# Kernel optimization log

Measured on AMD Instinct MI355X. Metric: run time of the kernel, lower is better.

The kernel has to match this reference:

```python
import jax, jax.numpy as jnp
import numpy as np

N_NODES = 50000
N_EDGES = 50000  # per-node attention scores are used as per-hyperedge weights => M == N
IN_CH = 128
OUT_CH = 128
NNZ = 800000


def setup_inputs() -> dict:
    key = jax.random.key(0)
    k = jax.random.split(key, 7)
    x = jax.random.normal(k[0], (N_NODES, IN_CH), dtype=jnp.float32)
    node_idx = jax.random.randint(k[1], (NNZ,), 0, N_NODES)
    edge_idx = jax.random.randint(k[2], (NNZ,), 0, N_EDGES)
    hyperedge_index = jnp.stack([node_idx, edge_idx]).astype(jnp.int64)
    s_in = 1.0 / np.sqrt(IN_CH)
    attn_w = jax.random.uniform(k[3], (1, IN_CH), minval=-s_in, maxval=s_in, dtype=jnp.float32)
    attn_b = jax.random.uniform(k[4], (1,), minval=-s_in, maxval=s_in, dtype=jnp.float32)
    lin_w = jax.random.uniform(k[5], (OUT_CH, IN_CH), minval=-s_in, maxval=s_in, dtype=jnp.float32)
    bias = jax.random.uniform(k[6], (OUT_CH,), minval=-s_in, maxval=s_in, dtype=jnp.float32)
    return {"x": x, "hyperedge_index": hyperedge_index,
            "attn_w": attn_w, "attn_b": attn_b, "lin_w": lin_w, "bias": bias}


def reference(x, hyperedge_index, attn_w, attn_b, lin_w, bias):
    # x: [N, C_in]; hyperedge_index: [2, nnz] (row 0: node ids, row 1: hyperedge ids)
    node_idx = hyperedge_index[0]
    edge_idx = hyperedge_index[1]
    N = x.shape[0]
    M = N_EDGES

    # edge_weight = sigmoid(attn(x)) -> used as hyperedge_weight (per-edge, M == N)
    w = jax.nn.sigmoid(x @ attn_w.T + attn_b)[:, 0]            # [M]

    xl = x @ lin_w.T                                           # [N, C_out]

    # D_v = sum of incident hyperedge weights per node; D^{-1} with inf -> 0
    D = jax.ops.segment_sum(w[edge_idx], node_idx, num_segments=N)
    Dinv = jnp.where(D > 0, 1.0 / D, 0.0)                      # [N]

    # B_e = hyperedge degree; B^{-1} with inf -> 0
    ones = jnp.ones(edge_idx.shape, dtype=x.dtype)
    Bdeg = jax.ops.segment_sum(ones, edge_idx, num_segments=M)
    Binv = jnp.where(Bdeg > 0, 1.0 / Bdeg, 0.0)                # [M]

    # node -> hyperedge: message = B_e^{-1} * x_j, aggregated at edge e
    msg = Binv[edge_idx][:, None] * xl[node_idx]               # [nnz, C_out]
    e_feat = jax.ops.segment_sum(msg, edge_idx, num_segments=M)

    # hyperedge -> node: message = D_v^{-1} * e_feat, aggregated at node v
    out = jax.ops.segment_sum(e_feat[edge_idx], node_idx, num_segments=N)
    out = Dinv[:, None] * out

    return out + bias
```

## Files before the change

### kernel.cpp

```cpp
#include <hip/hip_runtime.h>
#include <math.h>

#define CH 128
#define CAP 64
#define RSB 9
#define RS  (1 << RSB)
#define CAPB 10240
#define PB 2048
#define SUB 16
#define IDS 32

typedef __attribute__((ext_vector_type(8))) short bf16x8;
typedef __attribute__((ext_vector_type(4))) float f32x4;

__device__ __forceinline__ unsigned short f2bf(float f) {
    union { float f; unsigned u; } v; v.f = f;
    unsigned r = v.u + 0x7FFF + ((v.u >> 16) & 1);
    return (unsigned short)(r >> 16);
}
__device__ __forceinline__ float bflo(unsigned u) {
    union { unsigned u; float f; } v; v.u = u << 16; return v.f;
}
__device__ __forceinline__ float bfhi(unsigned u) {
    union { unsigned u; float f; } v; v.u = u & 0xFFFF0000u; return v.f;
}
__device__ __forceinline__ unsigned pack2bf(float a, float b) {
    return (unsigned)f2bf(a) | ((unsigned)f2bf(b) << 16);
}

__global__ __launch_bounds__(256) void fused_main(const float* __restrict__ x,
                                                  const float* __restrict__ attn_w,
                                                  const float* __restrict__ attn_b,
                                                  const float* __restrict__ lw,
                                                  unsigned short* __restrict__ xl,
                                                  float* __restrict__ w,
                                                  int nStrips,
                                                  const int* __restrict__ nidx,
                                                  const int* __restrict__ eidx,
                                                  int* __restrict__ binCnt,
                                                  unsigned int* __restrict__ binData,
                                                  int nnz, int nbd, int SB) {
    __shared__ unsigned short wl[128 * 136];
    __shared__ float awl[128];
    if ((int)blockIdx.x < SB) {
        int* hist = (int*)wl;
        int* base = ((int*)wl) + 256;
        int nbt = 2 * nbd;
        for (int i = threadIdx.x; i < nbt; i += 256) hist[i] = 0;
        __syncthreads();
        int k0 = blockIdx.x * PB + threadIdx.x;
        int vv[8], ee[8], sE[8], sN[8];
#pragma unroll
        for (int u = 0; u < 8; ++u) {
            int k = k0 + u * 256;
            if (k < nnz) {
                int v = nidx[k], e = eidx[k];
                vv[u] = v; ee[u] = e;
                sE[u] = atomicAdd(&hist[e >> RSB], 1);
                sN[u] = atomicAdd(&hist[nbd + (v >> RSB)], 1);
            } else vv[u] = -1;
        }
        __syncthreads();
        for (int i = threadIdx.x; i < nbt; i += 256)
            if (hist[i]) base[i] = atomicAdd(&binCnt[i], hist[i]);
        __syncthreads();
#pragma unroll
        for (int u = 0; u < 8; ++u) {
            if (vv[u] < 0) continue;
            int bE = ee[u] >> RSB;
            int bN = nbd + (vv[u] >> RSB);
            int iE = min(base[bE] + sE[u], CAPB - 1);
            int iN = min(base[bN] + sN[u], CAPB - 1);
            binData[(size_t)bE * CAPB + iE] = ((unsigned)ee[u] << 16) | (unsigned)vv[u];
            binData[(size_t)bN * CAPB + iN] = ((unsigned)vv[u] << 16) | (unsigned)ee[u];
        }
        return;
    }
    int tid = threadIdx.x;
    for (int i = tid; i < 2048; i += 256) {
        float4 vlo = ((const float4*)lw)[2 * i];
        float4 vhi = ((const float4*)lw)[2 * i + 1];
        int4 dst;
        dst.x = (int)pack2bf(vlo.x, vlo.y);
        dst.y = (int)pack2bf(vlo.z, vlo.w);
        dst.z = (int)pack2bf(vhi.x, vhi.y);
        dst.w = (int)pack2bf(vhi.z, vhi.w);
        *(int4*)(wl + (i >> 4) * 136 + (i & 15) * 8) = dst;
    }
    if (tid < 128) awl[tid] = attn_w[tid];
    float ab = attn_b[0];
    __syncthreads();
    int gb = blockIdx.x - SB;
    int wid = (gb << 2) | (tid >> 6);
    int lane = tid & 63;
    int m = lane & 15, quad = lane >> 4;
    int nWaves = ((int)gridDim.x - SB) << 2;
    for (int s = wid; s < nStrips; s += nWaves) {
        int r0 = s << 4;
        const float* xr = x + (size_t)(r0 + m) * CH + quad * 8;
        float att = 0.f;
        bf16x8 a0, a1, a2, a3;
#define LOAD_FRAG(AFRAG, F)                                                   \
        {                                                                     \
            float4 lo = *(const float4*)(xr + (F) * 32);                      \
            float4 hi = *(const float4*)(xr + (F) * 32 + 4);                  \
            const float* ap = &awl[(F) * 32 + quad * 8];                      \
            att += lo.x * ap[0] + lo.y * ap[1] + lo.z * ap[2] + lo.w * ap[3]  \
                 + hi.x * ap[4] + hi.y * ap[5] + hi.z * ap[6] + hi.w * ap[7]; \
            union { int4 i; bf16x8 v; } pk;                                   \
            pk.i.x = (int)pack2bf(lo.x, lo.y);                                \
            pk.i.y = (int)pack2bf(lo.z, lo.w);                                \
            pk.i.z = (int)pack2bf(hi.x, hi.y);                                \
            pk.i.w = (int)pack2bf(hi.z, hi.w);                                \
            AFRAG = pk.v;                                                     \
        }
        LOAD_FRAG(a0, 0)
        LOAD_FRAG(a1, 1)
        LOAD_FRAG(a2, 2)
        LOAD_FRAG(a3, 3)
#undef LOAD_FRAG
        att += __shfl_xor(att, 16, 64);
        att += __shfl_xor(att, 32, 64);
        if (quad == 0) w[r0 + m] = 1.0f / (1.0f + expf(-(att + ab)));
        unsigned short* orow = xl + (size_t)(r0 + quad * 4) * CH + m;
#pragma unroll
        for (int c0 = 0; c0 < 128; c0 += 16) {
            const unsigned short* wr = wl + (c0 + m) * 136 + quad * 8;
            f32x4 acc = {0.f, 0.f, 0.f, 0.f};
            acc = __builtin_amdgcn_mfma_f32_16x16x32_bf16(a0, *(const bf16x8*)(wr), acc, 0, 0, 0);
            acc = __builtin_amdgcn_mfma_f32_16x16x32_bf16(a1, *(const bf16x8*)(wr + 32), acc, 0, 0, 0);
            acc = __builtin_amdgcn_mfma_f32_16x16x32_bf16(a2, *(const bf16x8*)(wr + 64), acc, 0, 0, 0);
            acc = __builtin_amdgcn_mfma_f32_16x16x32_bf16(a3, *(const bf16x8*)(wr + 96), acc, 0, 0, 0);
            orow[c0]            = f2bf(acc[0]);
            orow[c0 + CH]       = f2bf(acc[1]);
            orow[c0 + 2 * CH]   = f2bf(acc[2]);
            orow[c0 + 3 * CH]   = f2bf(acc[3]);
        }
    }
}

__global__ __launch_bounds__(512, 8) void edge_agg(const int* __restrict__ binCnt,
                                                   const unsigned int* __restrict__ binData,
                                                   const unsigned short* __restrict__ xl,
                                                   unsigned short* __restrict__ ef, int M) {
    __shared__ unsigned short bucket[IDS * CAP];
    __shared__ int cl[IDS];
    int cb = blockIdx.x >> 4;
    int sr = blockIdx.x & (SUB - 1);
    int idBase = (cb << RSB) + (sr << 5);
    if (threadIdx.x < IDS) cl[threadIdx.x] = 0;
    __syncthreads();
    int n = min(binCnt[cb], CAPB);
    const unsigned int* src = binData + (size_t)cb * CAPB;
    for (int i0 = (int)threadIdx.x << 2; i0 < n; i0 += 2048) {
        if (i0 + 4 <= n) {
            uint4 e4 = *(const uint4*)(src + i0);
#define SCAN1(E) { int lid = (int)((E) >> 16) - idBase;                        \
                   if ((unsigned)lid < IDS) {                                  \
                       int r = atomicAdd(&cl[lid], 1);                         \
                       bucket[(lid << 6) + min(r, CAP - 1)] =                  \
                           (unsigned short)((E) & 0xFFFFu); } }
            SCAN1(e4.x) SCAN1(e4.y) SCAN1(e4.z) SCAN1(e4.w)
        } else {
            for (int i = i0; i < n; ++i) { unsigned int e1 = src[i]; SCAN1(e1) }
        }
    }
    __syncthreads();
    int wid = threadIdx.x >> 6, lane = threadIdx.x & 63;
    int half = lane >> 5, hl = lane & 31;
    for (int li = wid; li < IDS; li += 8) {
        int gid = idBase + li;
        if (gid >= M) break;
        int deg = cl[li];
        int dl = min(deg, CAP);
        const unsigned short* col = bucket + (li << 6);
        float4 acc = {0.f, 0.f, 0.f, 0.f};
        int npair = dl >> 1;
        int j = 0;
#define ROW(MID) { uint2 u = *(const uint2*)(xl + (size_t)(MID) * CH + 4 * hl); \
                   acc.x += bflo(u.x); acc.y += bfhi(u.x);                      \
                   acc.z += bflo(u.y); acc.w += bfhi(u.y); }
        for (; j + 4 <= npair; j += 4) {
            int m0 = col[2 * j + half];
            int m1 = col[2 * j + 2 + half];
            int m2 = col[2 * j + 4 + half];
            int m3 = col[2 * j + 6 + half];
            ROW(m0) ROW(m1) ROW(m2) ROW(m3)
        }
        for (; j < npair; ++j) { int m0 = col[2 * j + half]; ROW(m0) }
        if ((dl & 1) && half == 0) { int m0 = col[dl - 1]; ROW(m0) }
#undef ROW
        acc.x += __shfl_xor(acc.x, 32, 64);
        acc.y += __shfl_xor(acc.y, 32, 64);
        acc.z += __shfl_xor(acc.z, 32, 64);
        acc.w += __shfl_xor(acc.w, 32, 64);
        if (half == 0) {
            float binv = deg > 0 ? 1.0f / (float)deg : 0.0f;
            uint2 o;
            o.x = pack2bf(acc.x * binv, acc.y * binv);
            o.y = pack2bf(acc.z * binv, acc.w * binv);
            *(uint2*)(ef + (size_t)gid * CH + 4 * hl) = o;
        }
    }
}

__global__ __launch_bounds__(512, 8) void node_agg(const int* __restrict__ binCnt,
                                                   const unsigned int* __restrict__ binData,
                                                   const unsigned short* __restrict__ ef,
                                                   const float* __restrict__ w,
                                                   const float* __restrict__ bias,
                                                   float* __restrict__ out, int N) {
    __shared__ unsigned short bucket[IDS * CAP];
    __shared__ int cl[IDS];
    int cb = blockIdx.x >> 4;
    int sr = blockIdx.x & (SUB - 1);
    int idBase = (cb << RSB) + (sr << 5);
    if (threadIdx.x < IDS) cl[threadIdx.x] = 0;
    __syncthreads();
    int n = min(binCnt[cb], CAPB);
    const unsigned int* src = binData + (size_t)cb * CAPB;
    for (int i0 = (int)threadIdx.x << 2; i0 < n; i0 += 2048) {
        if (i0 + 4 <= n) {
            uint4 e4 = *(const uint4*)(src + i0);
            SCAN1(e4.x) SCAN1(e4.y) SCAN1(e4.z) SCAN1(e4.w)
        } else {
            for (int i = i0; i < n; ++i) { unsigned int e1 = src[i]; SCAN1(e1) }
        }
    }
#undef SCAN1
    __syncthreads();
    int wid = threadIdx.x >> 6, lane = threadIdx.x & 63;
    int half = lane >> 5, hl = lane & 31;
    for (int li = wid; li < IDS; li += 8) {
        int gid = idBase + li;
        if (gid >= N) break;
        int deg = cl[li];
        int dl = min(deg, CAP);
        const unsigned short* col = bucket + (li << 6);
        float4 acc = {0.f, 0.f, 0.f, 0.f};
        float ds = 0.f;
        int npair = dl >> 1;
        int j = 0;
#define ROW(MID) { uint2 u = *(const uint2*)(ef + (size_t)(MID) * CH + 4 * hl); \
                   ds += w[MID];                                                \
                   acc.x += bflo(u.x); acc.y += bfhi(u.x);                      \
                   acc.z += bflo(u.y); acc.w += bfhi(u.y); }
        for (; j + 4 <= npair; j += 4) {
            int m0 = col[2 * j + half];
            int m1 = col[2 * j + 2 + half];
            int m2 = col[2 * j + 4 + half];
            int m3 = col[2 * j + 6 + half];
            ROW(m0) ROW(m1) ROW(m2) ROW(m3)
        }
        for (; j < npair; ++j) { int m0 = col[2 * j + half]; ROW(m0) }
        if ((dl & 1) && half == 0) { int m0 = col[dl - 1]; ROW(m0) }
#undef ROW
        acc.x += __shfl_xor(acc.x, 32, 64);
        acc.y += __shfl_xor(acc.y, 32, 64);
        acc.z += __shfl_xor(acc.z, 32, 64);
        acc.w += __shfl_xor(acc.w, 32, 64);
        ds    += __shfl_xor(ds,    32, 64);
        if (half == 0) {
            float dinv = ds > 0.f ? 1.0f / ds : 0.0f;
            float4 bi = *(const float4*)(bias + 4 * hl);
            float4 o;
            o.x = acc.x * dinv + bi.x;
            o.y = acc.y * dinv + bi.y;
            o.z = acc.z * dinv + bi.z;
            o.w = acc.w * dinv + bi.w;
            *(float4*)(out + (size_t)gid * CH + 4 * hl) = o;
        }
    }
}

extern "C" void kernel_launch(void* const* d_in, const int* in_sizes, int n_in,
                              void* d_out, int out_size, void* d_ws, size_t ws_size,
                              hipStream_t stream) {
    const float* x      = (const float*)d_in[0];
    const int*   hei    = (const int*)d_in[1];
    const float* attn_w = (const float*)d_in[2];
    const float* attn_b = (const float*)d_in[3];
    const float* lin_w  = (const float*)d_in[4];
    const float* bias   = (const float*)d_in[5];
    float* out = (float*)d_out;

    const int N   = in_sizes[0] / CH;
    const int nnz = in_sizes[1] / 2;
    const int* nidx = hei;
    const int* eidx = hei + nnz;

    unsigned short* efbf = (unsigned short*)d_ws;
    float*          w    = (float*)(efbf + (size_t)N * CH);
    unsigned int*   binData = (unsigned int*)(w + N);
    int nbd = (N + RS - 1) >> RSB;
    int*            binCnt  = (int*)(binData + (size_t)2 * nbd * CAPB);

    unsigned short* xlbf = (unsigned short*)out;

    hipMemsetAsync(binCnt, 0, (size_t)2 * nbd * sizeof(int), stream);

    int SB = (nnz + PB - 1) / PB;
    int nStrips = N / 16;
    int GB = (nStrips + 3) / 4;
    fused_main<<<SB + GB, 256, 0, stream>>>(x, attn_w, attn_b, lin_w, xlbf, w,
                                            nStrips, nidx, eidx, binCnt, binData,
                                            nnz, nbd, SB);

    edge_agg<<<nbd * SUB, 512, 0, stream>>>(binCnt, binData, xlbf, efbf, N);
    node_agg<<<nbd * SUB, 512, 0, stream>>>(binCnt + nbd,
                                            binData + (size_t)nbd * CAPB,
                                            efbf, w, bias, out, N);
}
```

Baseline: 176.1 us.

## Store xl and edge features in column-chunked layout for cache-friendly gathers

The projected features and the per-hyperedge features are now stored as four 32-column chunks, each a contiguous [rows x 32] bf16 array, in place of row-major 128-wide rows. The gather kernels walk one chunk at a time, with each wave covering 8 neighbours per step using 8 lanes of 8 bytes each. The goal is to shrink the working set per pass so the random gathers hit L2/MALL more often. In exchange, the bucket lists are re-read four times, more shuffle reductions are needed, and each gathered row is only a 64-byte segment.

```diff
diff --git a/kernel.cpp b/kernel.cpp
--- a/kernel.cpp
+++ b/kernel.cpp
@@ -9,6 +9,7 @@
 #define PB 2048
 #define SUB 16
 #define IDS 32
+#define NCHUNK 4
 
 typedef __attribute__((ext_vector_type(8))) short bf16x8;
 typedef __attribute__((ext_vector_type(4))) float f32x4;
@@ -95,6 +96,7 @@
     int lane = tid & 63;
     int m = lane & 15, quad = lane >> 4;
     int nWaves = ((int)gridDim.x - SB) << 2;
+    size_t cs = (size_t)nStrips * 16 * 32;
     for (int s = wid; s < nStrips; s += nWaves) {
         int r0 = s << 4;
         const float* xr = x + (size_t)(r0 + m) * CH + quad * 8;
@@ -122,7 +124,7 @@
         att += __shfl_xor(att, 16, 64);
         att += __shfl_xor(att, 32, 64);
         if (quad == 0) w[r0 + m] = 1.0f / (1.0f + expf(-(att + ab)));
-        unsigned short* orow = xl + (size_t)(r0 + quad * 4) * CH + m;
+        unsigned short* ob = xl + (size_t)(r0 + quad * 4) * 32 + m;
 #pragma unroll
         for (int c0 = 0; c0 < 128; c0 += 16) {
             const unsigned short* wr = wl + (c0 + m) * 136 + quad * 8;
@@ -131,10 +133,11 @@
             acc = __builtin_amdgcn_mfma_f32_16x16x32_bf16(a1, *(const bf16x8*)(wr + 32), acc, 0, 0, 0);
             acc = __builtin_amdgcn_mfma_f32_16x16x32_bf16(a2, *(const bf16x8*)(wr + 64), acc, 0, 0, 0);
             acc = __builtin_amdgcn_mfma_f32_16x16x32_bf16(a3, *(const bf16x8*)(wr + 96), acc, 0, 0, 0);
-            orow[c0]            = f2bf(acc[0]);
-            orow[c0 + CH]       = f2bf(acc[1]);
-            orow[c0 + 2 * CH]   = f2bf(acc[2]);
-            orow[c0 + 3 * CH]   = f2bf(acc[3]);
+            unsigned short* oc = ob + (size_t)(c0 >> 5) * cs + (c0 & 16);
+            oc[0]   = f2bf(acc[0]);
+            oc[32]  = f2bf(acc[1]);
+            oc[64]  = f2bf(acc[2]);
+            oc[96]  = f2bf(acc[3]);
         }
     }
 }
@@ -142,7 +145,8 @@
 __global__ __launch_bounds__(512, 8) void edge_agg(const int* __restrict__ binCnt,
                                                    const unsigned int* __restrict__ binData,
                                                    const unsigned short* __restrict__ xl,
-                                                   unsigned short* __restrict__ ef, int M) {
+                                                   unsigned short* __restrict__ ef,
+                                                   int M, int rows) {
     __shared__ unsigned short bucket[IDS * CAP];
     __shared__ int cl[IDS];
     int cb = blockIdx.x >> 4;
@@ -152,54 +156,77 @@
     __syncthreads();
     int n = min(binCnt[cb], CAPB);
     const unsigned int* src = binData + (size_t)cb * CAPB;
-    for (int i0 = (int)threadIdx.x << 2; i0 < n; i0 += 2048) {
-        if (i0 + 4 <= n) {
-            uint4 e4 = *(const uint4*)(src + i0);
 #define SCAN1(E) { int lid = (int)((E) >> 16) - idBase;                        \
                    if ((unsigned)lid < IDS) {                                  \
                        int r = atomicAdd(&cl[lid], 1);                         \
                        bucket[(lid << 6) + min(r, CAP - 1)] =                  \
                            (unsigned short)((E) & 0xFFFFu); } }
+    for (int i0 = (int)threadIdx.x << 2; i0 < n; i0 += 2048) {
+        if (i0 + 4 <= n) {
+            uint4 e4 = *(const uint4*)(src + i0);
             SCAN1(e4.x) SCAN1(e4.y) SCAN1(e4.z) SCAN1(e4.w)
         } else {
             for (int i = i0; i < n; ++i) { unsigned int e1 = src[i]; SCAN1(e1) }
         }
     }
-    __syncthreads();
+#undef SCAN1
+    __syncthreads();
+    size_t cs = (size_t)rows * 32;
     int wid = threadIdx.x >> 6, lane = threadIdx.x & 63;
-    int half = lane >> 5, hl = lane & 31;
+    int g = lane >> 3, gl = lane & 7;
     for (int li = wid; li < IDS; li += 8) {
         int gid = idBase + li;
         if (gid >= M) break;
         int deg = cl[li];
         int dl = min(deg, CAP);
         const unsigned short* col = bucket + (li << 6);
-        float4 acc = {0.f, 0.f, 0.f, 0.f};
-        int npair = dl >> 1;
-        int j = 0;
-#define ROW(MID) { uint2 u = *(const uint2*)(xl + (size_t)(MID) * CH + 4 * hl); \
-                   acc.x += bflo(u.x); acc.y += bfhi(u.x);                      \
-                   acc.z += bflo(u.y); acc.w += bfhi(u.y); }
-        for (; j + 4 <= npair; j += 4) {
-            int m0 = col[2 * j + half];
-            int m1 = col[2 * j + 2 + half];
-            int m2 = col[2 * j + 4 + half];
-            int m3 = col[2 * j + 6 + half];
-            ROW(m0) ROW(m1) ROW(m2) ROW(m3)
-        }
-        for (; j < npair; ++j) { int m0 = col[2 * j + half]; ROW(m0) }
-        if ((dl & 1) && half == 0) { int m0 = col[dl - 1]; ROW(m0) }
-#undef ROW
-        acc.x += __shfl_xor(acc.x, 32, 64);
-        acc.y += __shfl_xor(acc.y, 32, 64);
-        acc.z += __shfl_xor(acc.z, 32, 64);
-        acc.w += __shfl_xor(acc.w, 32, 64);
-        if (half == 0) {
-            float binv = deg > 0 ? 1.0f / (float)deg : 0.0f;
-            uint2 o;
-            o.x = pack2bf(acc.x * binv, acc.y * binv);
-            o.y = pack2bf(acc.z * binv, acc.w * binv);
-            *(uint2*)(ef + (size_t)gid * CH + 4 * hl) = o;
+        float binv = deg > 0 ? 1.0f / (float)deg : 0.0f;
+#pragma unroll
+        for (int c = 0; c < NCHUNK; ++c) {
+            const unsigned short* bse = xl + (size_t)c * cs + (gl << 2);
+            float4 acc = {0.f, 0.f, 0.f, 0.f};
+            int j = 0;
+            for (; j + 16 <= dl; j += 16) {
+                int m0 = col[j + g], m1 = col[j + 8 + g];
+                uint2 u0 = *(const uint2*)(bse + (size_t)m0 * 32);
+                uint2 u1 = *(const uint2*)(bse + (size_t)m1 * 32);
+                acc.x += bflo(u0.x) + bflo(u1.x);
+                acc.y += bfhi(u0.x) + bfhi(u1.x);
+                acc.z += bflo(u0.y) + bflo(u1.y);
+                acc.w += bfhi(u0.y) + bfhi(u1.y);
+            }
+            if (j + 8 <= dl) {
+                int m0 = col[j + g];
+                uint2 u0 = *(const uint2*)(bse + (size_t)m0 * 32);
+                acc.x += bflo(u0.x); acc.y += bfhi(u0.x);
+                acc.z += bflo(u0.y); acc.w += bfhi(u0.y);
+                j += 8;
+            }
+            int rem = dl - j;
+            if (g < rem) {
+                int m0 = col[j + g];
+                uint2 u0 = *(const uint2*)(bse + (size_t)m0 * 32);
+                acc.x += bflo(u0.x); acc.y += bfhi(u0.x);
+                acc.z += bflo(u0.y); acc.w += bfhi(u0.y);
+            }
+            acc.x += __shfl_xor(acc.x, 8, 64);
+            acc.y += __shfl_xor(acc.y, 8, 64);
+            acc.z += __shfl_xor(acc.z, 8, 64);
+            acc.w += __shfl_xor(acc.w, 8, 64);
+            acc.x += __shfl_xor(acc.x, 16, 64);
+            acc.y += __shfl_xor(acc.y, 16, 64);
+            acc.z += __shfl_xor(acc.z, 16, 64);
+            acc.w += __shfl_xor(acc.w, 16, 64);
+            acc.x += __shfl_xor(acc.x, 32, 64);
+            acc.y += __shfl_xor(acc.y, 32, 64);
+            acc.z += __shfl_xor(acc.z, 32, 64);
+            acc.w += __shfl_xor(acc.w, 32, 64);
+            if (g == 0) {
+                uint2 o;
+                o.x = pack2bf(acc.x * binv, acc.y * binv);
+                o.y = pack2bf(acc.z * binv, acc.w * binv);
+                *(uint2*)(ef + (size_t)c * cs + (size_t)gid * 32 + (gl << 2)) = o;
+            }
         }
     }
 }
@@ -209,7 +236,8 @@
                                                    const unsigned short* __restrict__ ef,
                                                    const float* __restrict__ w,
                                                    const float* __restrict__ bias,
-                                                   float* __restrict__ out, int N) {
+                                                   float* __restrict__ out,
+                                                   int N, int rows) {
     __shared__ unsigned short bucket[IDS * CAP];
     __shared__ int cl[IDS];
     int cb = blockIdx.x >> 4;
@@ -219,6 +247,11 @@
     __syncthreads();
     int n = min(binCnt[cb], CAPB);
     const unsigned int* src = binData + (size_t)cb * CAPB;
+#define SCAN1(E) { int lid = (int)((E) >> 16) - idBase;                        \
+                   if ((unsigned)lid < IDS) {                                  \
+                       int r = atomicAdd(&cl[lid], 1);                         \
+                       bucket[(lid << 6) + min(r, CAP - 1)] =                  \
+                           (unsigned short)((E) & 0xFFFFu); } }
     for (int i0 = (int)threadIdx.x << 2; i0 < n; i0 += 2048) {
         if (i0 + 4 <= n) {
             uint4 e4 = *(const uint4*)(src + i0);
@@ -229,46 +262,75 @@
     }
 #undef SCAN1
     __syncthreads();
+    size_t cs = (size_t)rows * 32;
     int wid = threadIdx.x >> 6, lane = threadIdx.x & 63;
-    int half = lane >> 5, hl = lane & 31;
+    int g = lane >> 3, gl = lane & 7;
     for (int li = wid; li < IDS; li += 8) {
         int gid = idBase + li;
         if (gid >= N) break;
         int deg = cl[li];
         int dl = min(deg, CAP);
         const unsigned short* col = bucket + (li << 6);
-        float4 acc = {0.f, 0.f, 0.f, 0.f};
-        float ds = 0.f;
-        int npair = dl >> 1;
-        int j = 0;
-#define ROW(MID) { uint2 u = *(const uint2*)(ef + (size_t)(MID) * CH + 4 * hl); \
-                   ds += w[MID];                                                \
-                   acc.x += bflo(u.x); acc.y += bfhi(u.x);                      \
-                   acc.z += bflo(u.y); acc.w += bfhi(u.y); }
-        for (; j + 4 <= npair; j += 4) {
-            int m0 = col[2 * j + half];
-            int m1 = col[2 * j + 2 + half];
-            int m2 = col[2 * j + 4 + half];
-            int m3 = col[2 * j + 6 + half];
-            ROW(m0) ROW(m1) ROW(m2) ROW(m3)
-        }
-        for (; j < npair; ++j) { int m0 = col[2 * j + half]; ROW(m0) }
-        if ((dl & 1) && half == 0) { int m0 = col[dl - 1]; ROW(m0) }
-#undef ROW
-        acc.x += __shfl_xor(acc.x, 32, 64);
-        acc.y += __shfl_xor(acc.y, 32, 64);
-        acc.z += __shfl_xor(acc.z, 32, 64);
-        acc.w += __shfl_xor(acc.w, 32, 64);
-        ds    += __shfl_xor(ds,    32, 64);
-        if (half == 0) {
-            float dinv = ds > 0.f ? 1.0f / ds : 0.0f;
-            float4 bi = *(const float4*)(bias + 4 * hl);
-            float4 o;
-            o.x = acc.x * dinv + bi.x;
-            o.y = acc.y * dinv + bi.y;
-            o.z = acc.z * dinv + bi.z;
-            o.w = acc.w * dinv + bi.w;
-            *(float4*)(out + (size_t)gid * CH + 4 * hl) = o;
+        float dinv = 0.f;
+#pragma unroll
+        for (int c = 0; c < NCHUNK; ++c) {
+            const unsigned short* bse = ef + (size_t)c * cs + (gl << 2);
+            float4 acc = {0.f, 0.f, 0.f, 0.f};
+            float ds = 0.f;
+            int j = 0;
+            for (; j + 16 <= dl; j += 16) {
+                int m0 = col[j + g], m1 = col[j + 8 + g];
+                uint2 u0 = *(const uint2*)(bse + (size_t)m0 * 32);
+                uint2 u1 = *(const uint2*)(bse + (size_t)m1 * 32);
+                if (c == 0) ds += w[m0] + w[m1];
+                acc.x += bflo(u0.x) + bflo(u1.x);
+                acc.y += bfhi(u0.x) + bfhi(u1.x);
+                acc.z += bflo(u0.y) + bflo(u1.y);
+                acc.w += bfhi(u0.y) + bfhi(u1.y);
+            }
+            if (j + 8 <= dl) {
+                int m0 = col[j + g];
+                uint2 u0 = *(const uint2*)(bse + (size_t)m0 * 32);
+                if (c == 0) ds += w[m0];
+                acc.x += bflo(u0.x); acc.y += bfhi(u0.x);
+                acc.z += bflo(u0.y); acc.w += bfhi(u0.y);
+                j += 8;
+            }
+            int rem = dl - j;
+            if (g < rem) {
+                int m0 = col[j + g];
+                uint2 u0 = *(const uint2*)(bse + (size_t)m0 * 32);
+                if (c == 0) ds += w[m0];
+                acc.x += bflo(u0.x); acc.y += bfhi(u0.x);
+                acc.z += bflo(u0.y); acc.w += bfhi(u0.y);
+            }
+            acc.x += __shfl_xor(acc.x, 8, 64);
+            acc.y += __shfl_xor(acc.y, 8, 64);
+            acc.z += __shfl_xor(acc.z, 8, 64);
+            acc.w += __shfl_xor(acc.w, 8, 64);
+            acc.x += __shfl_xor(acc.x, 16, 64);
+            acc.y += __shfl_xor(acc.y, 16, 64);
+            acc.z += __shfl_xor(acc.z, 16, 64);
+            acc.w += __shfl_xor(acc.w, 16, 64);
+            acc.x += __shfl_xor(acc.x, 32, 64);
+            acc.y += __shfl_xor(acc.y, 32, 64);
+            acc.z += __shfl_xor(acc.z, 32, 64);
+            acc.w += __shfl_xor(acc.w, 32, 64);
+            if (c == 0) {
+                ds += __shfl_xor(ds, 8, 64);
+                ds += __shfl_xor(ds, 16, 64);
+                ds += __shfl_xor(ds, 32, 64);
+                dinv = ds > 0.f ? 1.0f / ds : 0.0f;
+            }
+            if (g == 0) {
+                float4 bi = *(const float4*)(bias + c * 32 + (gl << 2));
+                float4 o;
+                o.x = acc.x * dinv + bi.x;
+                o.y = acc.y * dinv + bi.y;
+                o.z = acc.z * dinv + bi.z;
+                o.w = acc.w * dinv + bi.w;
+                *(float4*)(out + (size_t)gid * CH + c * 32 + (gl << 2)) = o;
+            }
         }
     }
 }
@@ -306,8 +368,8 @@
                                             nStrips, nidx, eidx, binCnt, binData,
                                             nnz, nbd, SB);
 
-    edge_agg<<<nbd * SUB, 512, 0, stream>>>(binCnt, binData, xlbf, efbf, N);
+    edge_agg<<<nbd * SUB, 512, 0, stream>>>(binCnt, binData, xlbf, efbf, N, N);
     node_agg<<<nbd * SUB, 512, 0, stream>>>(binCnt + nbd,
                                             binData + (size_t)nbd * CAPB,
-                                            efbf, w, bias, out, N);
-}
+                                            efbf, w, bias, out, N, N);
+}
```

Measured after the change: 223.2 us. 1.27x slower.
